# Kernel optimization log

Hardware: AMD Instinct MI355X
Metric: run time of the kernel (lower is better)

## Reference

```python
import jax, jax.numpy as jnp
import numpy as np

N = 100000        # ncount
IN_C = 128        # in_channels
OUT_C = 64        # out_channels
S = 3             # number of wavelet scales
NNZ = 1_600_000   # nonzeros per sparse wavelet matrix (avg degree 16)
NNZ_F = 1_600_000 # nonzeros in sparse feature matrix


def spmm(indices, values, n_rows, dense):
    """Sparse [n_rows, *] COO matrix times dense matrix: out[r] += v * dense[c]."""
    rows, cols = indices[0], indices[1]
    return jax.ops.segment_sum(values[:, None] * dense[cols], rows, num_segments=n_rows)


def setup_inputs() -> dict:
    key = jax.random.key(0)
    ks = jax.random.split(key, 10)
    phi_indices = jax.random.randint(ks[0], (S, 2, NNZ), 0, N)
    phi_values = jax.random.uniform(ks[1], (S, NNZ), dtype=jnp.float32) * 0.1
    phi_inverse_indices = jax.random.randint(ks[2], (S, 2, NNZ), 0, N)
    phi_inverse_values = jax.random.uniform(ks[3], (S, NNZ), dtype=jnp.float32) * 0.1
    feat_rows = jax.random.randint(ks[4], (1, NNZ_F), 0, N)
    feat_cols = jax.random.randint(ks[5], (1, NNZ_F), 0, IN_C)
    feature_indices = jnp.concatenate([feat_rows, feat_cols], axis=0)
    feature_values = jax.random.uniform(ks[6], (NNZ_F,), dtype=jnp.float32)
    # xavier_uniform for weight_matrix
    bound = float(np.sqrt(6.0 / (IN_C + OUT_C)))
    weight_matrix = jax.random.uniform(ks[7], (IN_C, OUT_C), minval=-bound, maxval=bound, dtype=jnp.float32)
    # uniform(0.9, 1.1) diagonal filter (Theta)
    diagonal_weight_filter = jax.random.uniform(ks[8], (N, 1), minval=0.9, maxval=1.1, dtype=jnp.float32)
    return {
        'phi_indices': phi_indices,
        'phi_values': phi_values,
        'phi_inverse_indices': phi_inverse_indices,
        'phi_inverse_values': phi_inverse_values,
        'feature_indices': feature_indices,
        'feature_values': feature_values,
        'weight_matrix': weight_matrix,
        'diagonal_weight_filter': diagonal_weight_filter,
        'dropout': 0,  # eval mode: dropout is identity
    }


def reference(phi_indices, phi_values, phi_inverse_indices, phi_inverse_values,
              feature_indices, feature_values, weight_matrix, diagonal_weight_filter,
              dropout):
    # filtered = (sparse features) @ W   : [N, OUT_C]
    filtered = spmm(feature_indices, feature_values, N, weight_matrix)
    theta = diagonal_weight_filter[:, 0]  # [N]
    # Per scale: (phi @ diag(theta) @ phi_inv) @ filtered
    #          = phi @ (theta * (phi_inv @ filtered))   -- same math, no [N,N] product
    outs = []
    for i in range(S):  # fixed small number of scales
        z = spmm(phi_inverse_indices[i], phi_inverse_values[i], N, filtered)  # [N, OUT_C]
        z = theta[:, None] * z
        outs.append(spmm(phi_indices[i], phi_values[i], N, z))
    localized = jnp.stack(outs, axis=1)  # [N, S, OUT_C]
    # relu then dropout (eval: identity)
    return jax.nn.relu(localized)
```

## Files before the change

kernel.cpp:

```cpp
#include <hip/hip_runtime.h>
#include <hip/hip_bf16.h>

#define N_ROWS 100000
#define IN_C   128
#define OUT_C  64
#define S_SC   3
#define NNZ    1600000
#define NMAT   7

#define NCH    16
#define HROWS  (N_ROWS / 2)

#define SEG       512
#define BLKS_SCAN 196

#define NSEG   (NNZ / 256)
#define RPB    25000
#define NBIN_H 4

#define RPB_F  1024
#define NBKT   98
#define EPB_A  2048
#define BLKS_A ((NNZ + EPB_A - 1) / EPB_A)
#define RS_STR (N_ROWS + 1)

struct RowPtrs { const int* p[NMAT]; };

__device__ __forceinline__ float bf2f(__hip_bfloat16 x) { return __bfloat162float(x); }

__global__ __launch_bounds__(512)
void hist_binned(RowPtrs P, unsigned* __restrict__ counts16)
{
    __shared__ unsigned cnt[RPB / 2];
    const int m    = blockIdx.y;
    const int c    = blockIdx.x & (NCH - 1);
    const int bin0 = (blockIdx.x >> 4) * RPB;
    const int t    = threadIdx.x;

    for (int i = t; i < RPB / 2; i += 512) cnt[i] = 0;
    __syncthreads();

    const int* rows = P.p[m];
    const int wv = t >> 6;
    const int ln = t & 63;

    for (int sg = c + NCH * wv; sg < NSEG; sg += NCH * 8) {
        const int4 v = ((const int4*)rows)[sg * 64 + ln];
        unsigned i0 = (unsigned)(v.x - bin0);
        unsigned i1 = (unsigned)(v.y - bin0);
        unsigned i2 = (unsigned)(v.z - bin0);
        unsigned i3 = (unsigned)(v.w - bin0);
        if (i0 < RPB) atomicAdd(&cnt[i0 >> 1], 1u << ((i0 & 1) * 16));
        if (i1 < RPB) atomicAdd(&cnt[i1 >> 1], 1u << ((i1 & 1) * 16));
        if (i2 < RPB) atomicAdd(&cnt[i2 >> 1], 1u << ((i2 & 1) * 16));
        if (i3 < RPB) atomicAdd(&cnt[i3 >> 1], 1u << ((i3 & 1) * 16));
    }
    __syncthreads();

    unsigned* dst = counts16 + ((size_t)m * NCH + c) * HROWS + (bin0 >> 1);
    for (int i = t; i < RPB / 2; i += 512) dst[i] = cnt[i];
}

__global__ __launch_bounds__(256)
void scan_l1(const unsigned* __restrict__ counts16, int* __restrict__ rs,
             int* __restrict__ bsum)
{
    __shared__ int buf[2][SEG];
    const int m   = blockIdx.y;
    const int blk = blockIdx.x;
    const int t   = threadIdx.x;
    const unsigned* cnt = counts16 + (size_t)m * NCH * HROWS;

    for (int k = t; k < SEG; k += 256) {
        const int g = blk * SEG + k;
        int tot = 0;
        if (g < N_ROWS) {
            const int wi = g >> 1, sh = (g & 1) * 16;
            for (int c = 0; c < NCH; ++c)
                tot += (int)((cnt[(size_t)c * HROWS + wi] >> sh) & 0xffffu);
        }
        buf[0][k] = tot;
    }
    __syncthreads();

    int src = 0;
    for (int off = 1; off < SEG; off <<= 1) {
        for (int k = t; k < SEG; k += 256) {
            int v = buf[src][k];
            if (k >= off) v += buf[src][k - off];
            buf[1 - src][k] = v;
        }
        src ^= 1;
        __syncthreads();
    }
    for (int k = t; k < SEG; k += 256) {
        const int g = blk * SEG + k;
        if (g < N_ROWS)
            rs[(size_t)m * RS_STR + g] = (k == 0) ? 0 : buf[src][k - 1];
    }
    if (t == 0) bsum[m * 256 + blk] = buf[src][SEG - 1];
}

__global__ __launch_bounds__(256)
void scan_l2(int* __restrict__ bsum)
{
    __shared__ int buf[2][256];
    const int t = threadIdx.x;
    int* b = bsum + blockIdx.x * 256;
    buf[0][t] = (t < BLKS_SCAN) ? b[t] : 0;
    __syncthreads();
    int src = 0;
    for (int off = 1; off < 256; off <<= 1) {
        int v = buf[src][t];
        if (t >= off) v += buf[src][t - off];
        buf[1 - src][t] = v;
        src ^= 1;
        __syncthreads();
    }
    if (t < BLKS_SCAN) b[t] = (t == 0) ? 0 : buf[src][t - 1];
}

__global__ __launch_bounds__(256)
void finalize(const int* __restrict__ bsum, int* __restrict__ rs,
              int* __restrict__ bucket_cur)
{
    const int i = blockIdx.x * 256 + threadIdx.x;
    if (i >= NMAT * N_ROWS) return;
    const int m = i / N_ROWS;
    const int r = i - m * N_ROWS;
    const size_t ri = (size_t)m * RS_STR + r;
    const int base = rs[ri] + bsum[m * 256 + r / SEG];
    rs[ri] = base;
    if ((r & (RPB_F - 1)) == 0) bucket_cur[m * NBKT + (r >> 10)] = base;
    if (r == 0) rs[(size_t)m * RS_STR + N_ROWS] = NNZ;
}

__global__ __launch_bounds__(256)
void fill_a(const int* __restrict__ rows, const int* __restrict__ cols,
            const float* __restrict__ vals, int* __restrict__ bcur,
            uint2* __restrict__ bkt)
{
    __shared__ int cnt[NBKT], lofs[NBKT], lcur[NBKT], gbase[NBKT];
    __shared__ uint2 stg[EPB_A];
    __shared__ int gpos[EPB_A];
    const int t  = threadIdx.x;
    const int e0 = blockIdx.x * EPB_A;
    const int n  = min(EPB_A, NNZ - e0);

    for (int b = t; b < NBKT; b += 256) cnt[b] = 0;
    __syncthreads();

    int rr[8], cc[8], bb[8]; unsigned vv[8];
    #pragma unroll
    for (int k = 0; k < 8; ++k) {
        const int idx = t + k * 256;
        if (idx < n) {
            const int e = e0 + idx;
            rr[k] = rows[e];
            cc[k] = cols[e];
            vv[k] = __float_as_uint(vals[e]);
            bb[k] = rr[k] >> 10;
            atomicAdd(&cnt[bb[k]], 1);
        } else bb[k] = -1;
    }
    __syncthreads();

    if (t == 0) {
        int run = 0;
        for (int b = 0; b < NBKT; ++b) { lofs[b] = run; run += cnt[b]; }
    }
    __syncthreads();
    if (t < NBKT) {
        gbase[t] = atomicAdd(&bcur[t], cnt[t]);
        lcur[t]  = lofs[t];
    }
    __syncthreads();

    #pragma unroll
    for (int k = 0; k < 8; ++k) {
        if (bb[k] >= 0) {
            const int p = atomicAdd(&lcur[bb[k]], 1);
            stg[p]  = make_uint2(((unsigned)(rr[k] & (RPB_F - 1)) << 17) |
                                 (unsigned)cc[k], vv[k]);
            gpos[p] = gbase[bb[k]] + (p - lofs[bb[k]]);
        }
    }
    __syncthreads();

    for (int p = t; p < n; p += 256)
        bkt[gpos[p]] = stg[p];
}

__global__ __launch_bounds__(256)
void fill_b(const int* __restrict__ rs, const uint2* __restrict__ bkt,
            uint2* __restrict__ scv)
{
    __shared__ int cur[RPB_F];
    const int b  = blockIdx.x;
    const int r0 = b << 10;
    const int nr = min(RPB_F, N_ROWS - r0);
    const int t  = threadIdx.x;

    for (int i = t; i < nr; i += 256) cur[i] = rs[r0 + i];
    __syncthreads();

    const int e0 = rs[r0];
    const int e1 = rs[min(r0 + RPB_F, N_ROWS)];
    for (int e = e0 + t; e < e1; e += 256) {
        const uint2 rec = bkt[e];
        const int rl = (int)(rec.x >> 17);
        const int p  = atomicAdd(&cur[rl], 1);
        scv[p] = make_uint2(rec.x & 0x1FFFFu, rec.y);
    }
}

__global__ __launch_bounds__(256)
void gather_W(const int* __restrict__ rs, const uint2* __restrict__ scv,
              const float* __restrict__ W, __hip_bfloat16* __restrict__ dst)
{
    __shared__ float Wl[IN_C * OUT_C];
    for (int i = threadIdx.x; i < IN_C * OUT_C; i += blockDim.x) Wl[i] = W[i];
    __syncthreads();

    const int lane = threadIdx.x & 63;
    const int wave = blockIdx.x * 4 + (threadIdx.x >> 6);
    const int nw   = gridDim.x * 4;

    for (int r = wave; r < N_ROWS; r += nw) {
        const int s = rs[r], t = rs[r + 1];
        float a0 = 0.f, a1 = 0.f, a2 = 0.f, a3 = 0.f;
        float a4 = 0.f, a5 = 0.f, a6 = 0.f, a7 = 0.f;
        int j = s;
        for (; j + 7 < t; j += 8) {
            const uint2 p0 = scv[j],     p1 = scv[j + 1];
            const uint2 p2 = scv[j + 2], p3 = scv[j + 3];
            const uint2 p4 = scv[j + 4], p5 = scv[j + 5];
            const uint2 p6 = scv[j + 6], p7 = scv[j + 7];
            a0 += __uint_as_float(p0.y) * Wl[p0.x * OUT_C + lane];
            a1 += __uint_as_float(p1.y) * Wl[p1.x * OUT_C + lane];
            a2 += __uint_as_float(p2.y) * Wl[p2.x * OUT_C + lane];
            a3 += __uint_as_float(p3.y) * Wl[p3.x * OUT_C + lane];
            a4 += __uint_as_float(p4.y) * Wl[p4.x * OUT_C + lane];
            a5 += __uint_as_float(p5.y) * Wl[p5.x * OUT_C + lane];
            a6 += __uint_as_float(p6.y) * Wl[p6.x * OUT_C + lane];
            a7 += __uint_as_float(p7.y) * Wl[p7.x * OUT_C + lane];
        }
        for (; j + 3 < t; j += 4) {
            const uint2 p0 = scv[j],     p1 = scv[j + 1];
            const uint2 p2 = scv[j + 2], p3 = scv[j + 3];
            a0 += __uint_as_float(p0.y) * Wl[p0.x * OUT_C + lane];
            a1 += __uint_as_float(p1.y) * Wl[p1.x * OUT_C + lane];
            a2 += __uint_as_float(p2.y) * Wl[p2.x * OUT_C + lane];
            a3 += __uint_as_float(p3.y) * Wl[p3.x * OUT_C + lane];
        }
        for (; j < t; ++j) {
            const uint2 p = scv[j];
            a0 += __uint_as_float(p.y) * Wl[p.x * OUT_C + lane];
        }
        dst[(size_t)r * OUT_C + lane] =
            __float2bfloat16(((a0 + a1) + (a2 + a3)) + ((a4 + a5) + (a6 + a7)));
    }
}

template <int MODE>
__global__ __launch_bounds__(256)
void gather_mat(const int* __restrict__ rs, const uint2* __restrict__ scv,
                const __hip_bfloat16* __restrict__ src,
                const float* __restrict__ theta,
                __hip_bfloat16* __restrict__ dstb,
                float* __restrict__ dstf, int scale)
{
    const int lane = threadIdx.x & 63;
    const int wave = blockIdx.x * 4 + (threadIdx.x >> 6);
    const int nw   = gridDim.x * 4;

    for (int r = wave; r < N_ROWS; r += nw) {
        const int s = rs[r], t = rs[r + 1];
        float a0 = 0.f, a1 = 0.f, a2 = 0.f, a3 = 0.f;
        float a4 = 0.f, a5 = 0.f, a6 = 0.f, a7 = 0.f;
        int j = s;
        for (; j + 7 < t; j += 8) {
            const uint2 p0 = scv[j],     p1 = scv[j + 1];
            const uint2 p2 = scv[j + 2], p3 = scv[j + 3];
            const uint2 p4 = scv[j + 4], p5 = scv[j + 5];
            const uint2 p6 = scv[j + 6], p7 = scv[j + 7];
            const float w0 = bf2f(src[(size_t)p0.x * OUT_C + lane]);
            const float w1 = bf2f(src[(size_t)p1.x * OUT_C + lane]);
            const float w2 = bf2f(src[(size_t)p2.x * OUT_C + lane]);
            const float w3 = bf2f(src[(size_t)p3.x * OUT_C + lane]);
            const float w4 = bf2f(src[(size_t)p4.x * OUT_C + lane]);
            const float w5 = bf2f(src[(size_t)p5.x * OUT_C + lane]);
            const float w6 = bf2f(src[(size_t)p6.x * OUT_C + lane]);
            const float w7 = bf2f(src[(size_t)p7.x * OUT_C + lane]);
            a0 += __uint_as_float(p0.y) * w0;
            a1 += __uint_as_float(p1.y) * w1;
            a2 += __uint_as_float(p2.y) * w2;
            a3 += __uint_as_float(p3.y) * w3;
            a4 += __uint_as_float(p4.y) * w4;
            a5 += __uint_as_float(p5.y) * w5;
            a6 += __uint_as_float(p6.y) * w6;
            a7 += __uint_as_float(p7.y) * w7;
        }
        for (; j + 3 < t; j += 4) {
            const uint2 p0 = scv[j],     p1 = scv[j + 1];
            const uint2 p2 = scv[j + 2], p3 = scv[j + 3];
            const float w0 = bf2f(src[(size_t)p0.x * OUT_C + lane]);
            const float w1 = bf2f(src[(size_t)p1.x * OUT_C + lane]);
            const float w2 = bf2f(src[(size_t)p2.x * OUT_C + lane]);
            const float w3 = bf2f(src[(size_t)p3.x * OUT_C + lane]);
            a0 += __uint_as_float(p0.y) * w0;
            a1 += __uint_as_float(p1.y) * w1;
            a2 += __uint_as_float(p2.y) * w2;
            a3 += __uint_as_float(p3.y) * w3;
        }
        for (; j < t; ++j) {
            const uint2 p = scv[j];
            a0 += __uint_as_float(p.y) * bf2f(src[(size_t)p.x * OUT_C + lane]);
        }
        const float acc = ((a0 + a1) + (a2 + a3)) + ((a4 + a5) + (a6 + a7));
        if (MODE == 1) {
            dstb[(size_t)r * OUT_C + lane] = __float2bfloat16(theta[r] * acc);
        } else {
            dstf[((size_t)r * S_SC + scale) * OUT_C + lane] = acc > 0.0f ? acc : 0.0f;
        }
    }
}

extern "C" void kernel_launch(void* const* d_in, const int* in_sizes, int n_in,
                              void* d_out, int out_size, void* d_ws, size_t ws_size,
                              hipStream_t stream)
{
    const int*   phi_idx  = (const int*)d_in[0];
    const float* phi_val  = (const float*)d_in[1];
    const int*   pinv_idx = (const int*)d_in[2];
    const float* pinv_val = (const float*)d_in[3];
    const int*   fidx     = (const int*)d_in[4];
    const float* fval     = (const float*)d_in[5];
    const float* W        = (const float*)d_in[6];
    const float* theta    = (const float*)d_in[7];
    float*       out      = (float*)d_out;

    __hip_bfloat16* filtered = (__hip_bfloat16*)d_ws;
    __hip_bfloat16* z        = filtered + (size_t)N_ROWS * OUT_C;
    uint2* bkt = (uint2*)(z + (size_t)N_ROWS * OUT_C);
    uint2* scv = bkt + NNZ;
    unsigned* counts16 = (unsigned*)(scv + NNZ);
    int*   rs          = (int*)(counts16 + (size_t)NMAT * NCH * HROWS);
    int*   bsum        = rs + (size_t)NMAT * RS_STR;
    int*   bucket_cur  = bsum + NMAT * 256;

    RowPtrs P;
    P.p[0] = fidx;
    for (int i = 0; i < S_SC; ++i) {
        P.p[1 + 2 * i] = pinv_idx + (size_t)(2 * i) * NNZ;
        P.p[2 + 2 * i] = phi_idx  + (size_t)(2 * i) * NNZ;
    }

    hist_binned<<<dim3(NCH * NBIN_H, NMAT), 512, 0, stream>>>(P, counts16);
    scan_l1<<<dim3(BLKS_SCAN, NMAT), 256, 0, stream>>>(counts16, rs, bsum);
    scan_l2<<<NMAT, 256, 0, stream>>>(bsum);
    finalize<<<(NMAT * N_ROWS + 255) / 256, 256, 0, stream>>>(bsum, rs, bucket_cur);

    fill_a<<<BLKS_A, 256, 0, stream>>>(fidx, fidx + NNZ, fval, bucket_cur, bkt);
    fill_b<<<NBKT, 256, 0, stream>>>(rs, bkt, scv);
    gather_W<<<2048, 256, 0, stream>>>(rs, scv, W, filtered);

    for (int i = 0; i < S_SC; ++i) {
        const int m1 = 1 + 2 * i, m2 = 2 + 2 * i;
        const int*   zc = pinv_idx + (size_t)(2 * i + 1) * NNZ;
        const float* zv = pinv_val + (size_t)i * NNZ;
        const int*   oc = phi_idx  + (size_t)(2 * i + 1) * NNZ;
        const float* ov = phi_val  + (size_t)i * NNZ;

        fill_a<<<BLKS_A, 256, 0, stream>>>(P.p[m1], zc, zv,
                                           bucket_cur + m1 * NBKT, bkt);
        fill_b<<<NBKT, 256, 0, stream>>>(rs + (size_t)m1 * RS_STR, bkt, scv);
        gather_mat<1><<<4096, 256, 0, stream>>>(rs + (size_t)m1 * RS_STR, scv,
                                                filtered, theta, z, nullptr, 0);

        fill_a<<<BLKS_A, 256, 0, stream>>>(P.p[m2], oc, ov,
                                           bucket_cur + m2 * NBKT, bkt);
        fill_b<<<NBKT, 256, 0, stream>>>(rs + (size_t)m2 * RS_STR, bkt, scv);
        gather_mat<2><<<4096, 256, 0, stream>>>(rs + (size_t)m2 * RS_STR, scv,
                                                z, nullptr, nullptr, out, i);
    }
}
```

Measured before the change: 1.021 ms.

## Overlap next matrix's CSR fill with current gather via fused kernels

Merges the bucket-fill and scatter-fill work for the next sparse matrix into the same launches as the current matrix's SpMM gather. Each gather is split into two row halves, one co-launched with fill_a and one with fill_b, so the extra blocks run alongside the gather work. The scv buffer is double-buffered by reusing the histogram scratch space. This removes serialized fill phases and launch gaps, at the cost of splitting the gather across two launches and more LDS per block due to the union.

```diff
diff --git a/kernel.cpp b/kernel.cpp
--- a/kernel.cpp
+++ b/kernel.cpp
@@ -21,8 +21,11 @@
 #define RPB_F  1024
 #define NBKT   98
 #define EPB_A  2048
-#define BLKS_A ((NNZ + EPB_A - 1) / EPB_A)
+#define BLKS_A 782
 #define RS_STR (N_ROWS + 1)
+
+#define GH     2048
+#define RHALF  50000
 
 struct RowPtrs { const int* p[NMAT]; };
 
@@ -135,19 +138,22 @@
     if (r == 0) rs[(size_t)m * RS_STR + N_ROWS] = NNZ;
 }
 
-__global__ __launch_bounds__(256)
-void fill_a(const int* __restrict__ rows, const int* __restrict__ cols,
-            const float* __restrict__ vals, int* __restrict__ bcur,
-            uint2* __restrict__ bkt)
-{
-    __shared__ int cnt[NBKT], lofs[NBKT], lcur[NBKT], gbase[NBKT];
-    __shared__ uint2 stg[EPB_A];
-    __shared__ int gpos[EPB_A];
+struct FaLds {
+    int cnt[NBKT], lofs[NBKT], lcur[NBKT], gbase[NBKT];
+    uint2 stg[EPB_A];
+    int gpos[EPB_A];
+};
+
+__device__ __forceinline__ void fill_a_body(FaLds& L, int blk,
+    const int* __restrict__ rows, const int* __restrict__ cols,
+    const float* __restrict__ vals, int* __restrict__ bcur,
+    uint2* __restrict__ bkt)
+{
     const int t  = threadIdx.x;
-    const int e0 = blockIdx.x * EPB_A;
+    const int e0 = blk * EPB_A;
     const int n  = min(EPB_A, NNZ - e0);
 
-    for (int b = t; b < NBKT; b += 256) cnt[b] = 0;
+    for (int b = t; b < NBKT; b += 256) L.cnt[b] = 0;
     __syncthreads();
 
     int rr[8], cc[8], bb[8]; unsigned vv[8];
@@ -160,52 +166,49 @@
             cc[k] = cols[e];
             vv[k] = __float_as_uint(vals[e]);
             bb[k] = rr[k] >> 10;
-            atomicAdd(&cnt[bb[k]], 1);
+            atomicAdd(&L.cnt[bb[k]], 1);
         } else bb[k] = -1;
     }
     __syncthreads();
 
     if (t == 0) {
         int run = 0;
-        for (int b = 0; b < NBKT; ++b) { lofs[b] = run; run += cnt[b]; }
+        for (int b = 0; b < NBKT; ++b) { L.lofs[b] = run; run += L.cnt[b]; }
     }
     __syncthreads();
     if (t < NBKT) {
-        gbase[t] = atomicAdd(&bcur[t], cnt[t]);
-        lcur[t]  = lofs[t];
+        L.gbase[t] = atomicAdd(&bcur[t], L.cnt[t]);
+        L.lcur[t]  = L.lofs[t];
     }
     __syncthreads();
 
     #pragma unroll
     for (int k = 0; k < 8; ++k) {
         if (bb[k] >= 0) {
-            const int p = atomicAdd(&lcur[bb[k]], 1);
-            stg[p]  = make_uint2(((unsigned)(rr[k] & (RPB_F - 1)) << 17) |
-                                 (unsigned)cc[k], vv[k]);
-            gpos[p] = gbase[bb[k]] + (p - lofs[bb[k]]);
-        }
-    }
-    __syncthreads();
-
-    for (int p = t; p < n; p += 256)
-        bkt[gpos[p]] = stg[p];
-}
-
-__global__ __launch_bounds__(256)
-void fill_b(const int* __restrict__ rs, const uint2* __restrict__ bkt,
-            uint2* __restrict__ scv)
-{
-    __shared__ int cur[RPB_F];
-    const int b  = blockIdx.x;
+            const int p = atomicAdd(&L.lcur[bb[k]], 1);
+            L.stg[p]  = make_uint2(((unsigned)(rr[k] & (RPB_F - 1)) << 17) |
+                                   (unsigned)cc[k], vv[k]);
+            L.gpos[p] = L.gbase[bb[k]] + (p - L.lofs[bb[k]]);
+        }
+    }
+    __syncthreads();
+
+    for (int p = t; p < n; p += 256) bkt[L.gpos[p]] = L.stg[p];
+}
+
+__device__ __forceinline__ void fill_b_body(int* cur, int b,
+    const int* __restrict__ rs_m, const uint2* __restrict__ bkt,
+    uint2* __restrict__ scv)
+{
     const int r0 = b << 10;
     const int nr = min(RPB_F, N_ROWS - r0);
     const int t  = threadIdx.x;
 
-    for (int i = t; i < nr; i += 256) cur[i] = rs[r0 + i];
-    __syncthreads();
-
-    const int e0 = rs[r0];
-    const int e1 = rs[min(r0 + RPB_F, N_ROWS)];
+    for (int i = t; i < nr; i += 256) cur[i] = rs_m[r0 + i];
+    __syncthreads();
+
+    const int e0 = rs_m[r0];
+    const int e1 = rs_m[min(r0 + RPB_F, N_ROWS)];
     for (int e = e0 + t; e < e1; e += 256) {
         const uint2 rec = bkt[e];
         const int rl = (int)(rec.x >> 17);
@@ -215,19 +218,42 @@
 }
 
 __global__ __launch_bounds__(256)
-void gather_W(const int* __restrict__ rs, const uint2* __restrict__ scv,
-              const float* __restrict__ W, __hip_bfloat16* __restrict__ dst)
-{
-    __shared__ float Wl[IN_C * OUT_C];
-    for (int i = threadIdx.x; i < IN_C * OUT_C; i += blockDim.x) Wl[i] = W[i];
-    __syncthreads();
-
-    const int lane = threadIdx.x & 63;
-    const int wave = blockIdx.x * 4 + (threadIdx.x >> 6);
-    const int nw   = gridDim.x * 4;
-
-    for (int r = wave; r < N_ROWS; r += nw) {
-        const int s = rs[r], t = rs[r + 1];
+void fill_a(const int* __restrict__ rows, const int* __restrict__ cols,
+            const float* __restrict__ vals, int* __restrict__ bcur,
+            uint2* __restrict__ bkt)
+{
+    __shared__ FaLds L;
+    fill_a_body(L, blockIdx.x, rows, cols, vals, bcur, bkt);
+}
+
+__global__ __launch_bounds__(256)
+void fill_b(const int* __restrict__ rs_m, const uint2* __restrict__ bkt,
+            uint2* __restrict__ scv)
+{
+    __shared__ int cur[RPB_F];
+    fill_b_body(cur, blockIdx.x, rs_m, bkt, scv);
+}
+
+template <int GMODE>
+__device__ __forceinline__ float fetch_src(const float* Wl,
+                                           const __hip_bfloat16* src,
+                                           unsigned cx, int lane)
+{
+    if constexpr (GMODE == 0) return Wl[cx * OUT_C + lane];
+    else return bf2f(src[(size_t)cx * OUT_C + lane]);
+}
+
+template <int GMODE>
+__device__ __forceinline__ void gather_body(const float* Wl,
+    const int* __restrict__ rs_m, const uint2* __restrict__ scv,
+    const void* __restrict__ srcv, const float* __restrict__ theta,
+    __hip_bfloat16* __restrict__ dstb, float* __restrict__ dstf,
+    int scale, int r0, int r1, int wave, int nw, int lane)
+{
+    const __hip_bfloat16* src = (const __hip_bfloat16*)srcv;
+
+    for (int r = r0 + wave; r < r1; r += nw) {
+        const int s = rs_m[r], t = rs_m[r + 1];
         float a0 = 0.f, a1 = 0.f, a2 = 0.f, a3 = 0.f;
         float a4 = 0.f, a5 = 0.f, a6 = 0.f, a7 = 0.f;
         int j = s;
@@ -236,62 +262,14 @@
             const uint2 p2 = scv[j + 2], p3 = scv[j + 3];
             const uint2 p4 = scv[j + 4], p5 = scv[j + 5];
             const uint2 p6 = scv[j + 6], p7 = scv[j + 7];
-            a0 += __uint_as_float(p0.y) * Wl[p0.x * OUT_C + lane];
-            a1 += __uint_as_float(p1.y) * Wl[p1.x * OUT_C + lane];
-            a2 += __uint_as_float(p2.y) * Wl[p2.x * OUT_C + lane];
-            a3 += __uint_as_float(p3.y) * Wl[p3.x * OUT_C + lane];
-            a4 += __uint_as_float(p4.y) * Wl[p4.x * OUT_C + lane];
-            a5 += __uint_as_float(p5.y) * Wl[p5.x * OUT_C + lane];
-            a6 += __uint_as_float(p6.y) * Wl[p6.x * OUT_C + lane];
-            a7 += __uint_as_float(p7.y) * Wl[p7.x * OUT_C + lane];
-        }
-        for (; j + 3 < t; j += 4) {
-            const uint2 p0 = scv[j],     p1 = scv[j + 1];
-            const uint2 p2 = scv[j + 2], p3 = scv[j + 3];
-            a0 += __uint_as_float(p0.y) * Wl[p0.x * OUT_C + lane];
-            a1 += __uint_as_float(p1.y) * Wl[p1.x * OUT_C + lane];
-            a2 += __uint_as_float(p2.y) * Wl[p2.x * OUT_C + lane];
-            a3 += __uint_as_float(p3.y) * Wl[p3.x * OUT_C + lane];
-        }
-        for (; j < t; ++j) {
-            const uint2 p = scv[j];
-            a0 += __uint_as_float(p.y) * Wl[p.x * OUT_C + lane];
-        }
-        dst[(size_t)r * OUT_C + lane] =
-            __float2bfloat16(((a0 + a1) + (a2 + a3)) + ((a4 + a5) + (a6 + a7)));
-    }
-}
-
-template <int MODE>
-__global__ __launch_bounds__(256)
-void gather_mat(const int* __restrict__ rs, const uint2* __restrict__ scv,
-                const __hip_bfloat16* __restrict__ src,
-                const float* __restrict__ theta,
-                __hip_bfloat16* __restrict__ dstb,
-                float* __restrict__ dstf, int scale)
-{
-    const int lane = threadIdx.x & 63;
-    const int wave = blockIdx.x * 4 + (threadIdx.x >> 6);
-    const int nw   = gridDim.x * 4;
-
-    for (int r = wave; r < N_ROWS; r += nw) {
-        const int s = rs[r], t = rs[r + 1];
-        float a0 = 0.f, a1 = 0.f, a2 = 0.f, a3 = 0.f;
-        float a4 = 0.f, a5 = 0.f, a6 = 0.f, a7 = 0.f;
-        int j = s;
-        for (; j + 7 < t; j += 8) {
-            const uint2 p0 = scv[j],     p1 = scv[j + 1];
-            const uint2 p2 = scv[j + 2], p3 = scv[j + 3];
-            const uint2 p4 = scv[j + 4], p5 = scv[j + 5];
-            const uint2 p6 = scv[j + 6], p7 = scv[j + 7];
-            const float w0 = bf2f(src[(size_t)p0.x * OUT_C + lane]);
-            const float w1 = bf2f(src[(size_t)p1.x * OUT_C + lane]);
-            const float w2 = bf2f(src[(size_t)p2.x * OUT_C + lane]);
-            const float w3 = bf2f(src[(size_t)p3.x * OUT_C + lane]);
-            const float w4 = bf2f(src[(size_t)p4.x * OUT_C + lane]);
-            const float w5 = bf2f(src[(size_t)p5.x * OUT_C + lane]);
-            const float w6 = bf2f(src[(size_t)p6.x * OUT_C + lane]);
-            const float w7 = bf2f(src[(size_t)p7.x * OUT_C + lane]);
+            const float w0 = fetch_src<GMODE>(Wl, src, p0.x, lane);
+            const float w1 = fetch_src<GMODE>(Wl, src, p1.x, lane);
+            const float w2 = fetch_src<GMODE>(Wl, src, p2.x, lane);
+            const float w3 = fetch_src<GMODE>(Wl, src, p3.x, lane);
+            const float w4 = fetch_src<GMODE>(Wl, src, p4.x, lane);
+            const float w5 = fetch_src<GMODE>(Wl, src, p5.x, lane);
+            const float w6 = fetch_src<GMODE>(Wl, src, p6.x, lane);
+            const float w7 = fetch_src<GMODE>(Wl, src, p7.x, lane);
             a0 += __uint_as_float(p0.y) * w0;
             a1 += __uint_as_float(p1.y) * w1;
             a2 += __uint_as_float(p2.y) * w2;
@@ -304,10 +282,10 @@
         for (; j + 3 < t; j += 4) {
             const uint2 p0 = scv[j],     p1 = scv[j + 1];
             const uint2 p2 = scv[j + 2], p3 = scv[j + 3];
-            const float w0 = bf2f(src[(size_t)p0.x * OUT_C + lane]);
-            const float w1 = bf2f(src[(size_t)p1.x * OUT_C + lane]);
-            const float w2 = bf2f(src[(size_t)p2.x * OUT_C + lane]);
-            const float w3 = bf2f(src[(size_t)p3.x * OUT_C + lane]);
+            const float w0 = fetch_src<GMODE>(Wl, src, p0.x, lane);
+            const float w1 = fetch_src<GMODE>(Wl, src, p1.x, lane);
+            const float w2 = fetch_src<GMODE>(Wl, src, p2.x, lane);
+            const float w3 = fetch_src<GMODE>(Wl, src, p3.x, lane);
             a0 += __uint_as_float(p0.y) * w0;
             a1 += __uint_as_float(p1.y) * w1;
             a2 += __uint_as_float(p2.y) * w2;
@@ -315,15 +293,59 @@
         }
         for (; j < t; ++j) {
             const uint2 p = scv[j];
-            a0 += __uint_as_float(p.y) * bf2f(src[(size_t)p.x * OUT_C + lane]);
+            a0 += __uint_as_float(p.y) * fetch_src<GMODE>(Wl, src, p.x, lane);
         }
         const float acc = ((a0 + a1) + (a2 + a3)) + ((a4 + a5) + (a6 + a7));
-        if (MODE == 1) {
+        if (GMODE == 0) {
+            dstb[(size_t)r * OUT_C + lane] = __float2bfloat16(acc);
+        } else if (GMODE == 1) {
             dstb[(size_t)r * OUT_C + lane] = __float2bfloat16(theta[r] * acc);
         } else {
             dstf[((size_t)r * S_SC + scale) * OUT_C + lane] = acc > 0.0f ? acc : 0.0f;
         }
     }
+}
+
+template <int GMODE>
+__global__ __launch_bounds__(256)
+void fused_gf(int nFill, int fillKind,
+              const int* faRows, const int* faCols, const float* faVals,
+              int* faBcur,
+              const int* fbRs, uint2* bkt, uint2* fbScv,
+              const int* gRs, const uint2* gScv, const void* gSrc,
+              const float* theta, __hip_bfloat16* dstb, float* dstf,
+              int scale, int r0, int r1)
+{
+    constexpr int WLN = (GMODE == 0) ? (IN_C * OUT_C) : 1;
+    __shared__ union ULds {
+        FaLds fa;
+        int   fbcur[RPB_F];
+        float Wl[WLN];
+    } u;
+
+    const int t = threadIdx.x;
+    if ((int)blockIdx.x < nFill) {
+        if (fillKind == 1)
+            fill_a_body(u.fa, blockIdx.x, faRows, faCols, faVals, faBcur, bkt);
+        else
+            fill_b_body(u.fbcur, blockIdx.x, fbRs, bkt, fbScv);
+        return;
+    }
+
+    const int gb   = (int)blockIdx.x - nFill;
+    const int lane = t & 63;
+    const int wave = gb * 4 + (t >> 6);
+    const int nw   = ((int)gridDim.x - nFill) * 4;
+
+    const float* Wl = nullptr;
+    if constexpr (GMODE == 0) {
+        const float* W = (const float*)gSrc;
+        for (int i = t; i < IN_C * OUT_C; i += 256) u.Wl[i] = W[i];
+        __syncthreads();
+        Wl = u.Wl;
+    }
+    gather_body<GMODE>(Wl, gRs, gScv, gSrc, theta, dstb, dstf,
+                       scale, r0, r1, wave, nw, lane);
 }
 
 extern "C" void kernel_launch(void* const* d_in, const int* in_sizes, int n_in,
@@ -342,46 +364,90 @@
 
     __hip_bfloat16* filtered = (__hip_bfloat16*)d_ws;
     __hip_bfloat16* z        = filtered + (size_t)N_ROWS * OUT_C;
-    uint2* bkt = (uint2*)(z + (size_t)N_ROWS * OUT_C);
-    uint2* scv = bkt + NNZ;
-    unsigned* counts16 = (unsigned*)(scv + NNZ);
-    int*   rs          = (int*)(counts16 + (size_t)NMAT * NCH * HROWS);
-    int*   bsum        = rs + (size_t)NMAT * RS_STR;
-    int*   bucket_cur  = bsum + NMAT * 256;
+    uint2* bkt  = (uint2*)(z + (size_t)N_ROWS * OUT_C);
+    uint2* scv0 = bkt + NNZ;
+    unsigned* counts16 = (unsigned*)(scv0 + NNZ);
+    uint2* scv1 = (uint2*)counts16;
+    int*   rs         = (int*)(counts16 + (size_t)NMAT * NCH * HROWS);
+    int*   bsum       = rs + (size_t)NMAT * RS_STR;
+    int*   bucket_cur = bsum + NMAT * 256;
 
     RowPtrs P;
-    P.p[0] = fidx;
+    const int* kRows[NMAT]; const int* kCols[NMAT]; const float* kVals[NMAT];
+    kRows[0] = fidx; kCols[0] = fidx + NNZ; kVals[0] = fval;
     for (int i = 0; i < S_SC; ++i) {
-        P.p[1 + 2 * i] = pinv_idx + (size_t)(2 * i) * NNZ;
-        P.p[2 + 2 * i] = phi_idx  + (size_t)(2 * i) * NNZ;
-    }
+        kRows[1 + 2 * i] = pinv_idx + (size_t)(2 * i) * NNZ;
+        kCols[1 + 2 * i] = pinv_idx + (size_t)(2 * i + 1) * NNZ;
+        kVals[1 + 2 * i] = pinv_val + (size_t)i * NNZ;
+        kRows[2 + 2 * i] = phi_idx + (size_t)(2 * i) * NNZ;
+        kCols[2 + 2 * i] = phi_idx + (size_t)(2 * i + 1) * NNZ;
+        kVals[2 + 2 * i] = phi_val + (size_t)i * NNZ;
+    }
+    for (int k = 0; k < NMAT; ++k) P.p[k] = kRows[k];
 
     hist_binned<<<dim3(NCH * NBIN_H, NMAT), 512, 0, stream>>>(P, counts16);
     scan_l1<<<dim3(BLKS_SCAN, NMAT), 256, 0, stream>>>(counts16, rs, bsum);
     scan_l2<<<NMAT, 256, 0, stream>>>(bsum);
     finalize<<<(NMAT * N_ROWS + 255) / 256, 256, 0, stream>>>(bsum, rs, bucket_cur);
 
-    fill_a<<<BLKS_A, 256, 0, stream>>>(fidx, fidx + NNZ, fval, bucket_cur, bkt);
-    fill_b<<<NBKT, 256, 0, stream>>>(rs, bkt, scv);
-    gather_W<<<2048, 256, 0, stream>>>(rs, scv, W, filtered);
-
-    for (int i = 0; i < S_SC; ++i) {
-        const int m1 = 1 + 2 * i, m2 = 2 + 2 * i;
-        const int*   zc = pinv_idx + (size_t)(2 * i + 1) * NNZ;
-        const float* zv = pinv_val + (size_t)i * NNZ;
-        const int*   oc = phi_idx  + (size_t)(2 * i + 1) * NNZ;
-        const float* ov = phi_val  + (size_t)i * NNZ;
-
-        fill_a<<<BLKS_A, 256, 0, stream>>>(P.p[m1], zc, zv,
-                                           bucket_cur + m1 * NBKT, bkt);
-        fill_b<<<NBKT, 256, 0, stream>>>(rs + (size_t)m1 * RS_STR, bkt, scv);
-        gather_mat<1><<<4096, 256, 0, stream>>>(rs + (size_t)m1 * RS_STR, scv,
-                                                filtered, theta, z, nullptr, 0);
-
-        fill_a<<<BLKS_A, 256, 0, stream>>>(P.p[m2], oc, ov,
-                                           bucket_cur + m2 * NBKT, bkt);
-        fill_b<<<NBKT, 256, 0, stream>>>(rs + (size_t)m2 * RS_STR, bkt, scv);
-        gather_mat<2><<<4096, 256, 0, stream>>>(rs + (size_t)m2 * RS_STR, scv,
-                                                z, nullptr, nullptr, out, i);
-    }
-}
+    fill_a<<<BLKS_A, 256, 0, stream>>>(kRows[0], kCols[0], kVals[0],
+                                       bucket_cur, bkt);
+    fill_b<<<NBKT, 256, 0, stream>>>(rs, bkt, scv0);
+
+    for (int k = 0; k < NMAT; ++k) {
+        const uint2* gs   = (k & 1) ? scv1 : scv0;
+        const int*   grs  = rs + (size_t)k * RS_STR;
+        const void*  gsrc = (k == 0) ? (const void*)W
+                          : (k & 1)  ? (const void*)filtered : (const void*)z;
+        __hip_bfloat16* db = (k == 0) ? filtered : ((k & 1) ? z : nullptr);
+        const bool isOut = (k >= 2) && !(k & 1);
+        float* df = isOut ? out : nullptr;
+        const int sc = isOut ? (k - 2) / 2 : 0;
+        const int gm = (k == 0) ? 0 : ((k & 1) ? 1 : 2);
+
+        const int  kn      = k + 1;
+        const bool hasNext = kn < NMAT;
+        uint2* ns = (kn & 1) ? scv1 : scv0;
+
+        const int nFa = hasNext ? BLKS_A : 0;
+        const int nFb = hasNext ? NBKT : 0;
+
+        switch (gm) {
+        case 0: fused_gf<0><<<nFa + GH, 256, 0, stream>>>(nFa, 1,
+                    hasNext ? kRows[kn] : nullptr, hasNext ? kCols[kn] : nullptr,
+                    hasNext ? kVals[kn] : nullptr,
+                    hasNext ? bucket_cur + kn * NBKT : nullptr,
+                    nullptr, bkt, nullptr,
+                    grs, gs, gsrc, theta, db, df, sc, 0, RHALF); break;
+        case 1: fused_gf<1><<<nFa + GH, 256, 0, stream>>>(nFa, 1,
+                    hasNext ? kRows[kn] : nullptr, hasNext ? kCols[kn] : nullptr,
+                    hasNext ? kVals[kn] : nullptr,
+                    hasNext ? bucket_cur + kn * NBKT : nullptr,
+                    nullptr, bkt, nullptr,
+                    grs, gs, gsrc, theta, db, df, sc, 0, RHALF); break;
+        default: fused_gf<2><<<nFa + GH, 256, 0, stream>>>(nFa, 1,
+                    hasNext ? kRows[kn] : nullptr, hasNext ? kCols[kn] : nullptr,
+                    hasNext ? kVals[kn] : nullptr,
+                    hasNext ? bucket_cur + kn * NBKT : nullptr,
+                    nullptr, bkt, nullptr,
+                    grs, gs, gsrc, theta, db, df, sc, 0, RHALF); break;
+        }
+        switch (gm) {
+        case 0: fused_gf<0><<<nFb + GH, 256, 0, stream>>>(nFb, 2,
+                    nullptr, nullptr, nullptr, nullptr,
+                    hasNext ? rs + (size_t)kn * RS_STR : nullptr, bkt,
+                    hasNext ? ns : nullptr,
+                    grs, gs, gsrc, theta, db, df, sc, RHALF, N_ROWS); break;
+        case 1: fused_gf<1><<<nFb + GH, 256, 0, stream>>>(nFb, 2,
+                    nullptr, nullptr, nullptr, nullptr,
+                    hasNext ? rs + (size_t)kn * RS_STR : nullptr, bkt,
+                    hasNext ? ns : nullptr,
+                    grs, gs, gsrc, theta, db, df, sc, RHALF, N_ROWS); break;
+        default: fused_gf<2><<<nFb + GH, 256, 0, stream>>>(nFb, 2,
+                    nullptr, nullptr, nullptr, nullptr,
+                    hasNext ? rs + (size_t)kn * RS_STR : nullptr, bkt,
+                    hasNext ? ns : nullptr,
+                    grs, gs, gsrc, theta, db, df, sc, RHALF, N_ROWS); break;
+        }
+    }
+}
```

Result: no change. 1.011 ms (-1.0%).
